# Performance work log

Measured on AMD Instinct MI355X. Metric: run time of the kernel, lower is better.

## Reference

```python
import jax, jax.numpy as jnp
import numpy as np

B, T, D, H = 4, 2048, 1024, 16
HD = D // H  # 64


def setup_inputs() -> dict:
    key = jax.random.key(0)
    k1, k2, k3 = jax.random.split(key, 3)
    x = jax.random.normal(k1, (B, T, D), dtype=jnp.float32)
    # xavier-uniform-ish scaling for stability
    W_qkv = jax.random.normal(k2, (3 * D, D), dtype=jnp.float32) * (1.0 / np.sqrt(D))
    W_proj = jax.random.normal(k3, (D, D), dtype=jnp.float32) * (1.0 / np.sqrt(D))
    b_proj = jnp.zeros((D,), dtype=jnp.float32)
    return {"x": x, "W_qkv": W_qkv, "W_proj": W_proj, "b_proj": b_proj}


def reference(x, W_qkv, W_proj, b_proj):
    Bx, Tx, C = x.shape
    qkv = x @ W_qkv.T                      # [B,T,3C]
    q, k, v = jnp.split(qkv, 3, axis=-1)
    # [B,T,C] -> [B,H,T,hd]
    def heads(t):
        return t.reshape(Bx, Tx, H, HD).transpose(0, 2, 1, 3)
    q, k, v = heads(q), heads(k), heads(v)
    scale = 1.0 / np.sqrt(HD)
    scores = jnp.einsum('bhqd,bhkd->bhqk', q, k) * scale  # [B,H,T,T]
    causal = jnp.tril(jnp.ones((Tx, Tx), dtype=bool))
    scores = jnp.where(causal, scores, jnp.finfo(scores.dtype).min)
    attn = jax.nn.softmax(scores, axis=-1)
    out = jnp.einsum('bhqk,bhkd->bhqd', attn, v)          # [B,H,T,hd]
    out = out.transpose(0, 2, 1, 3).reshape(Bx, Tx, C)    # [B,T,C]
    return out @ W_proj.T + b_proj
```

## Files before the change

### kernel.cpp

```cpp
#include <hip/hip_runtime.h>
#include <hip/hip_bf16.h>

#define B_  4
#define T_  2048
#define D_  1024
#define H_  16
#define HD_ 64
#define THREE_D (3 * D_)

typedef short s16x8 __attribute__((ext_vector_type(8)));
typedef float f32x4 __attribute__((ext_vector_type(4)));
typedef unsigned short u16;
typedef unsigned short u16x4 __attribute__((ext_vector_type(4)));

static __device__ __forceinline__ s16x8 load8(const u16* p) {
    return *reinterpret_cast<const s16x8*>(p);
}
static __device__ __forceinline__ u16 f2bf(float f) {
    __hip_bfloat16 h = __float2bfloat16(f);
    return *reinterpret_cast<u16*>(&h);
}

static __device__ __forceinline__ void gload_lds16(const u16* g, u16* l) {
#if __has_builtin(__builtin_amdgcn_global_load_lds)
    __builtin_amdgcn_global_load_lds(
        (__attribute__((address_space(1))) void*)g,
        (__attribute__((address_space(3))) void*)l, 16, 0, 0);
#else
    *reinterpret_cast<s16x8*>(l) = load8(g);
#endif
}

__global__ __launch_bounds__(256) void cvt_f32_bf16(
    const float* __restrict__ in, u16* __restrict__ out, int n)
{
    const int i = (blockIdx.x * 256 + threadIdx.x) * 4;
    if (i < n) {
        const float4 f = *reinterpret_cast<const float4*>(in + i);
        u16x4 r;
        r.x = f2bf(f.x); r.y = f2bf(f.y); r.z = f2bf(f.z); r.w = f2bf(f.w);
        *reinterpret_cast<u16x4*>(out + i) = r;
    }
}

template<bool OUT_BF16>
__global__ __launch_bounds__(256) void gemm_bt128(
    const u16* __restrict__ A,
    const u16* __restrict__ Bm,
    void* __restrict__ Cv,
    const float* __restrict__ bias,
    int M, int N, int K, int lda, int ldb, int ldc)
{
    const int ntiles = N >> 7;
    const int mt = blockIdx.x / ntiles;
    const int nt = blockIdx.x % ntiles;
    const int m0 = mt * 128, n0 = nt * 128;
    const int tid  = threadIdx.x;
    const int lane = tid & 63;
    const int l15  = lane & 15;
    const int quad = lane >> 4;
    const int wave = tid >> 6;
    const int wm = (wave >> 1) * 64;
    const int wn = (wave & 1) * 64;

    __shared__ u16 A_sh[2][128 * 32];
    __shared__ u16 B_sh[2][128 * 32];

    f32x4 acc[4][4] = {};

    const int c0 = tid, c1 = tid + 256;
    const int ar0 = c0 >> 2, as0 = (c0 & 3) * 8;
    const int ar1 = c1 >> 2, as1 = (c1 & 3) * 8;
    const u16* Ag0 = A  + (size_t)(m0 + ar0) * lda + as0;
    const u16* Ag1 = A  + (size_t)(m0 + ar1) * lda + as1;
    const u16* Bg0 = Bm + (size_t)(n0 + ar0) * ldb + as0;
    const u16* Bg1 = Bm + (size_t)(n0 + ar1) * ldb + as1;

    for (int k0 = 0; k0 < K; k0 += 64) {
        __syncthreads();
        #pragma unroll
        for (int p = 0; p < 2; ++p) {
            gload_lds16(Ag0 + k0 + p * 32, &A_sh[p][c0 * 8]);
            gload_lds16(Ag1 + k0 + p * 32, &A_sh[p][c1 * 8]);
            gload_lds16(Bg0 + k0 + p * 32, &B_sh[p][c0 * 8]);
            gload_lds16(Bg1 + k0 + p * 32, &B_sh[p][c1 * 8]);
        }
        __syncthreads();

        #pragma unroll
        for (int p = 0; p < 2; ++p) {
            s16x8 a[4], b[4];
            #pragma unroll
            for (int i = 0; i < 4; ++i) {
                a[i] = *reinterpret_cast<const s16x8*>(&A_sh[p][(wm + i * 16 + l15) * 32 + quad * 8]);
                b[i] = *reinterpret_cast<const s16x8*>(&B_sh[p][(wn + i * 16 + l15) * 32 + quad * 8]);
            }
            #pragma unroll
            for (int mi = 0; mi < 4; ++mi)
                #pragma unroll
                for (int ni = 0; ni < 4; ++ni)
                    acc[mi][ni] = __builtin_amdgcn_mfma_f32_16x16x32_bf16(
                        a[mi], b[ni], acc[mi][ni], 0, 0, 0);
        }
    }

    #pragma unroll
    for (int ni = 0; ni < 4; ++ni) {
        const int col = n0 + wn + ni * 16 + l15;
        const float bv = bias ? bias[col] : 0.0f;
        #pragma unroll
        for (int mi = 0; mi < 4; ++mi) {
            const int row = m0 + wm + mi * 16 + quad * 4;
            #pragma unroll
            for (int r = 0; r < 4; ++r) {
                if (OUT_BF16)
                    ((u16*)Cv)[(size_t)(row + r) * ldc + col] = f2bf(acc[mi][ni][r] + bv);
                else
                    ((float*)Cv)[(size_t)(row + r) * ldc + col] = acc[mi][ni][r] + bv;
            }
        }
    }
}

__global__ __launch_bounds__(256) void transpose_v(
    const u16* __restrict__ qkv, u16* __restrict__ vt)
{
    const int nt = T_ / 64;
    const int tt = blockIdx.x % nt;
    const int bh = blockIdx.x / nt;
    const int t0 = tt * 64;
    __shared__ u16 tileT[64 * 72];
    const int tid = threadIdx.x;

    #pragma unroll
    for (int it = 0; it < 2; ++it) {
        const int c = tid + it * 256;
        const int t = c >> 3, fsub = c & 7;
        const s16x8 v = load8(qkv + (size_t)((bh >> 4) * T_ + t0 + t) * THREE_D
                                  + 2 * D_ + (bh & 15) * HD_ + fsub * 8);
        #pragma unroll
        for (int j = 0; j < 8; ++j)
            tileT[(fsub * 8 + j) * 72 + (t ^ (fsub << 3))] = (u16)v[j];
    }
    __syncthreads();
    #pragma unroll
    for (int it = 0; it < 2; ++it) {
        const int c = tid + it * 256;
        const int f = c >> 3, sub = c & 7;
        const s16x8 v = *reinterpret_cast<const s16x8*>(
            &tileT[f * 72 + ((sub ^ ((f >> 3) & 7)) << 3)]);
        *reinterpret_cast<s16x8*>(vt + (size_t)(bh * HD_ + f) * T_ + t0 + sub * 8) = v;
    }
}

__global__ __launch_bounds__(256) void flash_attn3(
    const u16* __restrict__ qkv, const u16* __restrict__ vt,
    u16* __restrict__ out)
{
    const int cls = blockIdx.x >> 6;
    const int bh  = blockIdx.x & 63;
    const int qmap[16] = {15,14,13,12, 8,9,10,11, 7,6,5,4, 0,1,2,3};
    const int qt = qmap[cls];
    const int h = bh & 15, b = bh >> 4;
    const int q0 = qt * 128;

    __shared__ u16 K_lds[64 * 72];
    __shared__ u16 P_lds[4 * 32 * 72];

    const int tid = threadIdx.x;
    const int wave = tid >> 6, lane = tid & 63;
    const int l15 = lane & 15, quad = lane >> 4;
    u16* Pw = P_lds + wave * (32 * 72);

    const int w0 = q0 + wave * 32;

    s16x8 qf[2][2];
    #pragma unroll
    for (int mi = 0; mi < 2; ++mi) {
        const size_t rowQ = (size_t)(b * T_ + w0 + mi * 16 + l15) * THREE_D + h * HD_;
        qf[mi][0] = load8(qkv + rowQ + quad * 8);
        qf[mi][1] = load8(qkv + rowQ + 32 + quad * 8);
    }

    f32x4 o[2][4] = {};
    f32x4 osum[2] = {};

    const float cs = 0.18033688011f;
    s16x8 ones;
    #pragma unroll
    for (int j = 0; j < 8; ++j) ones[j] = (short)0x3F80;

    const u16* Kg = qkv + (size_t)(b * T_) * THREE_D + D_ + h * HD_;
    const u16* Vg = vt + (size_t)bh * HD_ * T_;

    const int nkt = 2 * qt + 2;
    for (int kt = 0; kt < nkt; ++kt) {
        const int kbase = kt * 64;
        __syncthreads();
        #pragma unroll
        for (int it = 0; it < 2; ++it) {
            const int c = tid + it * 256;
            const int row = c >> 3, sub = c & 7;
            *reinterpret_cast<s16x8*>(&K_lds[row * 72 + sub * 8]) =
                load8(Kg + (size_t)(kbase + row) * THREE_D + sub * 8);
        }
        __syncthreads();

        if (kbase <= w0 + 31) {
            s16x8 kf[4][2];
            #pragma unroll
            for (int n = 0; n < 4; ++n) {
                kf[n][0] = *reinterpret_cast<const s16x8*>(&K_lds[(n * 16 + l15) * 72 + quad * 8]);
                kf[n][1] = *reinterpret_cast<const s16x8*>(&K_lds[(n * 16 + l15) * 72 + 32 + quad * 8]);
            }
            s16x8 vb[4][2];
            #pragma unroll
            for (int n4 = 0; n4 < 4; ++n4) {
                const u16* vr = Vg + (size_t)(n4 * 16 + l15) * T_ + kbase;
                vb[n4][0] = load8(vr + quad * 8);
                vb[n4][1] = load8(vr + 32 + quad * 8);
            }

            const bool diag = (kbase + 63 > w0);
            #pragma unroll
            for (int mi = 0; mi < 2; ++mi) {
                f32x4 s[4];
                #pragma unroll
                for (int n = 0; n < 4; ++n) {
                    f32x4 t = {};
                    t = __builtin_amdgcn_mfma_f32_16x16x32_bf16(qf[mi][0], kf[n][0], t, 0, 0, 0);
                    t = __builtin_amdgcn_mfma_f32_16x16x32_bf16(qf[mi][1], kf[n][1], t, 0, 0, 0);
                    s[n] = t;
                }
                const int rbase = mi * 16 + quad * 4;
                if (diag) {
                    #pragma unroll
                    for (int r = 0; r < 4; ++r) {
                        const int qr = w0 + mi * 16 + quad * 4 + r;
                        #pragma unroll
                        for (int n = 0; n < 4; ++n) {
                            const u16 p = (kbase + n * 16 + l15 > qr)
                                        ? (u16)0 : f2bf(exp2f(s[n][r] * cs));
                            Pw[(rbase + r) * 72 + n * 16 + l15] = p;
                        }
                    }
                } else {
                    #pragma unroll
                    for (int r = 0; r < 4; ++r)
                        #pragma unroll
                        for (int n = 0; n < 4; ++n)
                            Pw[(rbase + r) * 72 + n * 16 + l15] = f2bf(exp2f(s[n][r] * cs));
                }

                #pragma unroll
                for (int ks = 0; ks < 2; ++ks) {
                    const s16x8 pa = *reinterpret_cast<const s16x8*>(
                        &Pw[(mi * 16 + l15) * 72 + ks * 32 + quad * 8]);
                    osum[mi] = __builtin_amdgcn_mfma_f32_16x16x32_bf16(pa, ones, osum[mi], 0, 0, 0);
                    #pragma unroll
                    for (int n4 = 0; n4 < 4; ++n4)
                        o[mi][n4] = __builtin_amdgcn_mfma_f32_16x16x32_bf16(
                            pa, vb[n4][ks], o[mi][n4], 0, 0, 0);
                }
            }
        }
    }

    #pragma unroll
    for (int mi = 0; mi < 2; ++mi)
        #pragma unroll
        for (int r = 0; r < 4; ++r) {
            const float inv = 1.0f / osum[mi][r];
            const size_t rowO = (size_t)(b * T_ + w0 + mi * 16 + quad * 4 + r) * D_ + h * HD_;
            #pragma unroll
            for (int n4 = 0; n4 < 4; ++n4)
                out[rowO + n4 * 16 + l15] = f2bf(o[mi][n4][r] * inv);
        }
}

extern "C" void kernel_launch(void* const* d_in, const int* in_sizes, int n_in,
                              void* d_out, int out_size, void* d_ws, size_t ws_size,
                              hipStream_t stream)
{
    const float* x     = (const float*)d_in[0];
    const float* Wqkv  = (const float*)d_in[1];
    const float* Wproj = (const float*)d_in[2];
    const float* bproj = (const float*)d_in[3];
    float* out = (float*)d_out;

    const int M = B_ * T_;

    u16* xb    = (u16*)d_ws;
    u16* wqkvb = xb    + (size_t)M * D_;
    u16* wprob = wqkvb + (size_t)THREE_D * D_;
    u16* qkv   = wprob + (size_t)D_ * D_;
    u16* attn  = qkv   + (size_t)M * THREE_D;
    u16* vtb   = xb;

    {
        int n;
        n = M * D_;
        cvt_f32_bf16<<<dim3((n / 4 + 255) / 256), 256, 0, stream>>>(x, xb, n);
        n = THREE_D * D_;
        cvt_f32_bf16<<<dim3((n / 4 + 255) / 256), 256, 0, stream>>>(Wqkv, wqkvb, n);
        n = D_ * D_;
        cvt_f32_bf16<<<dim3((n / 4 + 255) / 256), 256, 0, stream>>>(Wproj, wprob, n);
    }

    gemm_bt128<true><<<dim3((M / 128) * (THREE_D / 128)), 256, 0, stream>>>(
        xb, wqkvb, qkv, nullptr, M, THREE_D, D_, D_, D_, THREE_D);

    transpose_v<<<dim3(B_ * H_ * (T_ / 64)), 256, 0, stream>>>(qkv, vtb);

    flash_attn3<<<dim3(B_ * H_ * (T_ / 128)), 256, 0, stream>>>(qkv, vtb, attn);

    gemm_bt128<false><<<dim3((M / 128) * (D_ / 128)), 256, 0, stream>>>(
        attn, wprob, out, bproj, M, D_, D_, D_, D_, D_);
}
```

Baseline: 287.9 us.

## Drop K LDS staging, fold softmax scale into QKV GEMM, per-wave tile counts

The attention kernel now loads K fragments straight from global memory into registers instead of staging them through shared memory. This removes both __syncthreads per key tile and lets each wave loop only over its own causal range (w0/64+1 tiles). The softmax scale times log2e is folded into the Q columns in the QKV GEMM epilogue, so exp2 needs no per-element multiply, and bf16 rounding of P is replaced by truncation. The risks are redundant global K loads across the four waves, a small precision change from scaling Q before bf16 rounding and from truncating P, and no max subtraction, which the old code also lacked.

```diff
diff --git a/kernel.cpp b/kernel.cpp
--- a/kernel.cpp
+++ b/kernel.cpp
@@ -19,6 +19,9 @@
 static __device__ __forceinline__ u16 f2bf(float f) {
     __hip_bfloat16 h = __float2bfloat16(f);
     return *reinterpret_cast<u16*>(&h);
+}
+static __device__ __forceinline__ u16 bftrunc(float f) {
+    unsigned u; __builtin_memcpy(&u, &f, 4); return (u16)(u >> 16);
 }
 
 static __device__ __forceinline__ void gload_lds16(const u16* g, u16* l) {
@@ -49,7 +52,8 @@
     const u16* __restrict__ Bm,
     void* __restrict__ Cv,
     const float* __restrict__ bias,
-    int M, int N, int K, int lda, int ldb, int ldc)
+    int M, int N, int K, int lda, int ldb, int ldc,
+    int qcols, float qsc)
 {
     const int ntiles = N >> 7;
     const int mt = blockIdx.x / ntiles;
@@ -108,15 +112,16 @@
     for (int ni = 0; ni < 4; ++ni) {
         const int col = n0 + wn + ni * 16 + l15;
         const float bv = bias ? bias[col] : 0.0f;
+        const float sc = (col < qcols) ? qsc : 1.0f;
         #pragma unroll
         for (int mi = 0; mi < 4; ++mi) {
             const int row = m0 + wm + mi * 16 + quad * 4;
             #pragma unroll
             for (int r = 0; r < 4; ++r) {
                 if (OUT_BF16)
-                    ((u16*)Cv)[(size_t)(row + r) * ldc + col] = f2bf(acc[mi][ni][r] + bv);
+                    ((u16*)Cv)[(size_t)(row + r) * ldc + col] = f2bf(acc[mi][ni][r] * sc + bv);
                 else
-                    ((float*)Cv)[(size_t)(row + r) * ldc + col] = acc[mi][ni][r] + bv;
+                    ((float*)Cv)[(size_t)(row + r) * ldc + col] = acc[mi][ni][r] * sc + bv;
             }
         }
     }
@@ -153,7 +158,7 @@
     }
 }
 
-__global__ __launch_bounds__(256) void flash_attn3(
+__global__ __launch_bounds__(256) void flash_attn4(
     const u16* __restrict__ qkv, const u16* __restrict__ vt,
     u16* __restrict__ out)
 {
@@ -164,7 +169,6 @@
     const int h = bh & 15, b = bh >> 4;
     const int q0 = qt * 128;
 
-    __shared__ u16 K_lds[64 * 72];
     __shared__ u16 P_lds[4 * 32 * 72];
 
     const int tid = threadIdx.x;
@@ -185,7 +189,6 @@
     f32x4 o[2][4] = {};
     f32x4 osum[2] = {};
 
-    const float cs = 0.18033688011f;
     s16x8 ones;
     #pragma unroll
     for (int j = 0; j < 8; ++j) ones[j] = (short)0x3F80;
@@ -193,75 +196,67 @@
     const u16* Kg = qkv + (size_t)(b * T_) * THREE_D + D_ + h * HD_;
     const u16* Vg = vt + (size_t)bh * HD_ * T_;
 
-    const int nkt = 2 * qt + 2;
+    const int nkt = (w0 >> 6) + 1;
     for (int kt = 0; kt < nkt; ++kt) {
         const int kbase = kt * 64;
-        __syncthreads();
-        #pragma unroll
-        for (int it = 0; it < 2; ++it) {
-            const int c = tid + it * 256;
-            const int row = c >> 3, sub = c & 7;
-            *reinterpret_cast<s16x8*>(&K_lds[row * 72 + sub * 8]) =
-                load8(Kg + (size_t)(kbase + row) * THREE_D + sub * 8);
-        }
-        __syncthreads();
-
-        if (kbase <= w0 + 31) {
-            s16x8 kf[4][2];
-            #pragma unroll
-            for (int n = 0; n < 4; ++n) {
-                kf[n][0] = *reinterpret_cast<const s16x8*>(&K_lds[(n * 16 + l15) * 72 + quad * 8]);
-                kf[n][1] = *reinterpret_cast<const s16x8*>(&K_lds[(n * 16 + l15) * 72 + 32 + quad * 8]);
-            }
-            s16x8 vb[4][2];
+
+        f32x4 s[2][4];
+        #pragma unroll
+        for (int n = 0; n < 4; ++n) {
+            const u16* kr = Kg + (size_t)(kbase + n * 16 + l15) * THREE_D;
+            const s16x8 kf0 = load8(kr + quad * 8);
+            const s16x8 kf1 = load8(kr + 32 + quad * 8);
+            #pragma unroll
+            for (int mi = 0; mi < 2; ++mi) {
+                f32x4 t = {};
+                t = __builtin_amdgcn_mfma_f32_16x16x32_bf16(qf[mi][0], kf0, t, 0, 0, 0);
+                t = __builtin_amdgcn_mfma_f32_16x16x32_bf16(qf[mi][1], kf1, t, 0, 0, 0);
+                s[mi][n] = t;
+            }
+        }
+
+        if (kt == nkt - 1) {
+            #pragma unroll
+            for (int mi = 0; mi < 2; ++mi)
+                #pragma unroll
+                for (int r = 0; r < 4; ++r) {
+                    const int qr = w0 + mi * 16 + quad * 4 + r;
+                    #pragma unroll
+                    for (int n = 0; n < 4; ++n) {
+                        const u16 p = (kbase + n * 16 + l15 > qr)
+                                    ? (u16)0 : bftrunc(exp2f(s[mi][n][r]));
+                        Pw[(mi * 16 + quad * 4 + r) * 72 + n * 16 + l15] = p;
+                    }
+                }
+        } else {
+            #pragma unroll
+            for (int mi = 0; mi < 2; ++mi)
+                #pragma unroll
+                for (int r = 0; r < 4; ++r)
+                    #pragma unroll
+                    for (int n = 0; n < 4; ++n)
+                        Pw[(mi * 16 + quad * 4 + r) * 72 + n * 16 + l15] =
+                            bftrunc(exp2f(s[mi][n][r]));
+        }
+
+        #pragma unroll
+        for (int ks = 0; ks < 2; ++ks) {
+            s16x8 pa[2];
+            #pragma unroll
+            for (int mi = 0; mi < 2; ++mi) {
+                pa[mi] = *reinterpret_cast<const s16x8*>(
+                    &Pw[(mi * 16 + l15) * 72 + ks * 32 + quad * 8]);
+                osum[mi] = __builtin_amdgcn_mfma_f32_16x16x32_bf16(
+                    pa[mi], ones, osum[mi], 0, 0, 0);
+            }
             #pragma unroll
             for (int n4 = 0; n4 < 4; ++n4) {
-                const u16* vr = Vg + (size_t)(n4 * 16 + l15) * T_ + kbase;
-                vb[n4][0] = load8(vr + quad * 8);
-                vb[n4][1] = load8(vr + 32 + quad * 8);
-            }
-
-            const bool diag = (kbase + 63 > w0);
-            #pragma unroll
-            for (int mi = 0; mi < 2; ++mi) {
-                f32x4 s[4];
+                const s16x8 vb = load8(Vg + (size_t)(n4 * 16 + l15) * T_
+                                       + kbase + ks * 32 + quad * 8);
                 #pragma unroll
-                for (int n = 0; n < 4; ++n) {
-                    f32x4 t = {};
-                    t = __builtin_amdgcn_mfma_f32_16x16x32_bf16(qf[mi][0], kf[n][0], t, 0, 0, 0);
-                    t = __builtin_amdgcn_mfma_f32_16x16x32_bf16(qf[mi][1], kf[n][1], t, 0, 0, 0);
-                    s[n] = t;
-                }
-                const int rbase = mi * 16 + quad * 4;
-                if (diag) {
-                    #pragma unroll
-                    for (int r = 0; r < 4; ++r) {
-                        const int qr = w0 + mi * 16 + quad * 4 + r;
-                        #pragma unroll
-                        for (int n = 0; n < 4; ++n) {
-                            const u16 p = (kbase + n * 16 + l15 > qr)
-                                        ? (u16)0 : f2bf(exp2f(s[n][r] * cs));
-                            Pw[(rbase + r) * 72 + n * 16 + l15] = p;
-                        }
-                    }
-                } else {
-                    #pragma unroll
-                    for (int r = 0; r < 4; ++r)
-                        #pragma unroll
-                        for (int n = 0; n < 4; ++n)
-                            Pw[(rbase + r) * 72 + n * 16 + l15] = f2bf(exp2f(s[n][r] * cs));
-                }
-
-                #pragma unroll
-                for (int ks = 0; ks < 2; ++ks) {
-                    const s16x8 pa = *reinterpret_cast<const s16x8*>(
-                        &Pw[(mi * 16 + l15) * 72 + ks * 32 + quad * 8]);
-                    osum[mi] = __builtin_amdgcn_mfma_f32_16x16x32_bf16(pa, ones, osum[mi], 0, 0, 0);
-                    #pragma unroll
-                    for (int n4 = 0; n4 < 4; ++n4)
-                        o[mi][n4] = __builtin_amdgcn_mfma_f32_16x16x32_bf16(
-                            pa, vb[n4][ks], o[mi][n4], 0, 0, 0);
-                }
+                for (int mi = 0; mi < 2; ++mi)
+                    o[mi][n4] = __builtin_amdgcn_mfma_f32_16x16x32_bf16(
+                        pa[mi], vb, o[mi][n4], 0, 0, 0);
             }
         }
     }
@@ -289,6 +284,7 @@
     float* out = (float*)d_out;
 
     const int M = B_ * T_;
+    const float cs = 0.18033688011f;
 
     u16* xb    = (u16*)d_ws;
     u16* wqkvb = xb    + (size_t)M * D_;
@@ -308,12 +304,12 @@
     }
 
     gemm_bt128<true><<<dim3((M / 128) * (THREE_D / 128)), 256, 0, stream>>>(
-        xb, wqkvb, qkv, nullptr, M, THREE_D, D_, D_, D_, THREE_D);
+        xb, wqkvb, qkv, nullptr, M, THREE_D, D_, D_, D_, THREE_D, D_, cs);
 
     transpose_v<<<dim3(B_ * H_ * (T_ / 64)), 256, 0, stream>>>(qkv, vtb);
 
-    flash_attn3<<<dim3(B_ * H_ * (T_ / 128)), 256, 0, stream>>>(qkv, vtb, attn);
+    flash_attn4<<<dim3(B_ * H_ * (T_ / 128)), 256, 0, stream>>>(qkv, vtb, attn);
 
     gemm_bt128<false><<<dim3((M / 128) * (D_ / 128)), 256, 0, stream>>>(
-        attn, wprob, out, bproj, M, D_, D_, D_, D_, D_);
-}
+        attn, wprob, out, bproj, M, D_, D_, D_, D_, D_, 0, 1.0f);
+}
```

Result: slower. 346.8 us (+20.5%).
